# Performance work log

Measured on AMD Instinct MI355X. Metric: run time of the kernel, lower is better.

The kernel has to match this reference:

```python
import jax, jax.numpy as jnp
import numpy as np

PI = np.float32(np.pi)

def _normalize(x, eps=1e-6):
    # matches torch F.normalize: x / max(||x||, eps)
    return x / jnp.maximum(jnp.linalg.norm(x, axis=-1, keepdims=True), eps)

def _linear2srgb(x, eps=1e-8):
    lin = 12.92 * x
    exp = 1.055 * jnp.power(jnp.maximum(x, eps), 1.0 / 2.4) - 0.055
    return jnp.where(x <= 0.0031308, lin, exp)

def _ggx_specular(nrm, surf2c, surf2l, roughness, fresnel):
    # nrm [N,3], surf2c [N,3], surf2l [1,L,3] (unit), roughness [N,1], fresnel [N,3]
    L = _normalize(surf2l)                                  # [1,L,3]
    V = _normalize(surf2c)                                  # [N,3]
    H = _normalize((L + V[:, None, :]) / 2.0)               # [N,L,3]
    N = _normalize(nrm)                                     # [N,3]
    NoV = jnp.sum(V * N, axis=-1, keepdims=True)            # [N,1]
    N = N * jnp.sign(NoV)
    NoL = jnp.clip(jnp.sum(N[:, None, :] * L, axis=-1, keepdims=True), 1e-6, 1.0)  # [N,L,1]
    NoV = jnp.clip(jnp.sum(N * V, axis=-1, keepdims=True), 1e-6, 1.0)              # [N,1]
    NoH = jnp.clip(jnp.sum(N[:, None, :] * H, axis=-1, keepdims=True), 1e-6, 1.0)  # [N,L,1]
    VoH = jnp.clip(jnp.sum(V[:, None, :] * H, axis=-1, keepdims=True), 1e-6, 1.0)  # [N,L,1]
    alpha = roughness * roughness                            # [N,1]
    alpha2 = alpha * alpha
    k = (alpha + 2.0 * roughness + 1.0) / 8.0                # [N,1]
    FMi = ((-5.55473) * VoH - 6.98316) * VoH                 # [N,L,1]
    frac0 = fresnel[:, None, :] + (1.0 - fresnel[:, None, :]) * jnp.power(2.0, FMi)  # [N,L,3]
    frac = frac0 * alpha2[:, None, :]                        # [N,L,3]
    nom0 = NoH * NoH * (alpha2[:, None, :] - 1.0) + 1.0      # [N,L,1]
    nom1 = NoV[:, None, :] * (1.0 - k[:, None, :]) + k[:, None, :]  # [N,1,1]
    nom2 = NoL * (1.0 - k[:, None, :]) + k[:, None, :]       # [N,L,1]
    nom = jnp.clip(4.0 * PI * nom0 * nom0 * nom1 * nom2, 1e-6, 4.0 * PI)
    return frac / nom                                        # [N,L,3]

def setup_inputs() -> dict:
    key = jax.random.key(0)
    ks = jax.random.split(key, 9)
    N, L = 32768, 512
    f32 = jnp.float32
    return {
        'viewdirs': jax.random.normal(ks[0], (N, 3), f32),
        'albedo': jax.random.uniform(ks[1], (N, 3), dtype=f32),
        'roughness': jax.random.uniform(ks[2], (N, 1), dtype=f32),
        'fresnel': jnp.full((N, 3), 0.04, dtype=f32),
        'normal': jax.random.normal(ks[3], (N, 3), f32),
        'light_dirs': jax.random.normal(ks[4], (L, 3), f32),
        'light_area_weight': jax.random.uniform(ks[5], (L,), dtype=f32),
        'env_rgbs': jax.random.uniform(ks[6], (L, 3), dtype=f32),
        'visibility': jax.random.uniform(ks[7], (N, L, 1), dtype=f32),
        'indirect_light': jax.random.uniform(ks[8], (N, L, 3), dtype=f32),
    }

def reference(viewdirs, albedo, roughness, fresnel, normal, light_dirs,
              light_area_weight, env_rgbs, visibility, indirect_light):
    # sample(): albedo clamp, roughness affine+clamp, normal normalize
    albedo = jnp.clip(albedo, 0.0, 1.0)
    roughness = jnp.clip(roughness * 0.9 + 0.09, 0.0, 1.0)
    nrm = _normalize(normal)
    surf2l = _normalize(light_dirs)[None, :, :]              # [1,L,3]
    surf2c = _normalize(-viewdirs)                            # [N,3]
    cosine = jnp.clip(jnp.einsum('lk,nk->nl', _normalize(light_dirs), nrm), 0.0)  # [N,L]
    mask = (cosine > 1e-6)[..., None]                         # [N,L,1]
    vis = visibility * mask                                   # scatter-into-zeros equivalent
    ind = indirect_light * mask
    spec = _ggx_specular(nrm, surf2c, surf2l, roughness, fresnel)  # [N,L,3]
    brdf = albedo[:, None, :] / PI + spec                      # [N,L,3]
    direct = env_rgbs[None, :, :]                              # [1,L,3] (light_idx all zero)
    w = cosine[..., None] * light_area_weight[None, :, None]   # [N,L,1]
    light_rgbs = vis * direct + ind
    rgb = _linear2srgb(jnp.clip(jnp.sum(brdf * light_rgbs * w, axis=1), 0.0, 1.0))
    wo_indir = _linear2srgb(jnp.sum(brdf * (vis * direct) * w, axis=1))
    wo_vis = _linear2srgb(jnp.sum(brdf * direct * w, axis=1))
    indir = _linear2srgb(jnp.sum(brdf * ind * w, axis=1))
    return rgb, wo_indir, wo_vis, indir
```

## Files before the change

kernel.cpp:

```cpp
#include <hip/hip_runtime.h>
#include <math.h>


#define PI_F     3.14159265358979323846f
#define FOURPI_F (4.0f * PI_F)
#define MAXL     512

__device__ __forceinline__ float fast_rcp(float x)  { float r; asm("v_rcp_f32 %0, %1" : "=v"(r) : "v"(x)); return r; }
__device__ __forceinline__ float fast_rsq(float x)  { float r; asm("v_rsq_f32 %0, %1" : "=v"(r) : "v"(x)); return r; }
__device__ __forceinline__ float fast_exp2(float x) { float r; asm("v_exp_f32 %0, %1" : "=v"(r) : "v"(x)); return r; }
__device__ __forceinline__ float fast_log2(float x) { float r; asm("v_log_f32 %0, %1" : "=v"(r) : "v"(x)); return r; }

__device__ __forceinline__ float lin2srgb(float x) {
  float lin = 12.92f * x;
  float xe  = fmaxf(x, 1e-8f);
  float e   = 1.055f * fast_exp2(fast_log2(xe) * (1.0f / 2.4f)) - 0.055f;
  return (x <= 0.0031308f) ? lin : e;
}

__device__ __forceinline__ float clamp01(float x) { return fminf(fmaxf(x, 0.0f), 1.0f); }
__device__ __forceinline__ float clampe(float x)  { return fminf(fmaxf(x, 1e-6f), 1.0f); }

template <int LC>
__global__ void __launch_bounds__(256)
tensoir_render(const float* __restrict__ viewdirs,
               const float* __restrict__ albedo,
               const float* __restrict__ roughness,
               const float* __restrict__ fresnel,
               const float* __restrict__ normal,
               const float* __restrict__ light_dirs,
               const float* __restrict__ law,
               const float* __restrict__ env_rgbs,
               const float* __restrict__ visibility,
               const float* __restrict__ indirect,
               float* __restrict__ out,
               int N, int Lrt) {
  __shared__ float4 s_ld[MAXL];
  __shared__ float4 s_env[MAXL];

  const int L = LC ? LC : Lrt;
  const int tid = threadIdx.x;
  const int lane = tid & 63;
  int n = blockIdx.x * 4 + (tid >> 6);
  if (n >= N) n = N - 1;

  float vx = -viewdirs[3 * n + 0], vy = -viewdirs[3 * n + 1], vz = -viewdirs[3 * n + 2];
  float nx = normal[3 * n + 0], ny = normal[3 * n + 1], nz = normal[3 * n + 2];
  float rough0 = roughness[n];
  const float fr = fresnel[3 * n + 0], fg = fresnel[3 * n + 1], fb = fresnel[3 * n + 2];
  float ar0 = albedo[3 * n + 0], ag0 = albedo[3 * n + 1], ab0 = albedo[3 * n + 2];

  for (int l = tid; l < L && l < MAXL; l += 256) {
    float lx = light_dirs[3 * l + 0];
    float ly = light_dirs[3 * l + 1];
    float lz = light_dirs[3 * l + 2];
    float inv = fast_rsq(fmaxf(lx * lx + ly * ly + lz * lz, 1e-12f));
    s_ld[l]  = make_float4(lx * inv, ly * inv, lz * inv, law[l]);
    s_env[l] = make_float4(env_rgbs[3 * l + 0], env_rgbs[3 * l + 1],
                           env_rgbs[3 * l + 2], 0.0f);
  }
  __syncthreads();

  {
    float inv = fast_rsq(fmaxf(vx * vx + vy * vy + vz * vz, 1e-12f));
    vx *= inv; vy *= inv; vz *= inv;
  }
  {
    float inv = fast_rsq(fmaxf(nx * nx + ny * ny + nz * nz, 1e-12f));
    nx *= inv; ny *= inv; nz *= inv;
  }
  const float rough  = clamp01(rough0 * 0.9f + 0.09f);
  const float alpha  = rough * rough;
  const float alpha2 = alpha * alpha;
  const float a2m1   = alpha2 - 1.0f;
  const float kk     = (alpha + 2.0f * rough + 1.0f) * 0.125f;
  const float onemk  = 1.0f - kk;

  const float omfr = 1.0f - fr, omfg = 1.0f - fg, omfb = 1.0f - fb;
  const float ar = clamp01(ar0) * (1.0f / PI_F);
  const float ag = clamp01(ag0) * (1.0f / PI_F);
  const float ab = clamp01(ab0) * (1.0f / PI_F);

  const float NoV0 = vx * nx + vy * ny + vz * nz;
  const float sgn  = (NoV0 >= 0.0f) ? 1.0f : -1.0f;
  const float aNoV = fabsf(NoV0);
  const float NoV  = clampe(aNoV);
  const float nom1 = NoV * onemk + kk;
  const float c1   = FOURPI_F * nom1;

  float s1r = 0, s1g = 0, s1b = 0;
  float s2r = 0, s2g = 0, s2b = 0;
  float s3r = 0, s3g = 0, s3b = 0;

  const float* visrow = visibility + (size_t)n * L;
  const float* indrow = indirect + (size_t)n * L * 3;

  auto body = [&](int i) {
    const float4 ld = s_ld[i];
    const float4 ev = s_env[i];
    const float visv = visrow[i];
    const float ir = indrow[3 * i + 0];
    const float ig = indrow[3 * i + 1];
    const float ib = indrow[3 * i + 2];

    const float cos0 = ld.x * nx + ld.y * ny + ld.z * nz;
    const float LoV  = ld.x * vx + ld.y * vy + ld.z * vz;

    const float cosine = fmaxf(cos0, 0.0f);
    const bool  mask   = cos0 > 1e-6f;
    const float w      = cosine * ld.w;

    const float NoL0 = sgn * cos0;
    const float NoL  = clampe(NoL0);

    const float h2   = fmaf(2.0f, LoV, 2.0f);
    const float hinv = fast_rsq(fmaxf(h2, 1e-12f));
    const float VoH  = clampe((1.0f + LoV) * hinv);
    const float NoH  = clampe((NoL0 + aNoV) * hinv);

    const float FMi = (-5.55473f * VoH - 6.98316f) * VoH;
    const float p2  = fast_exp2(FMi);
    const float nom0 = fmaf(NoH * NoH, a2m1, 1.0f);
    const float nom2 = fmaf(NoL, onemk, kk);
    const float nom  = fminf(fmaxf(c1 * (nom0 * nom0) * nom2, 1e-6f), FOURPI_F);
    const float ss   = alpha2 * fast_rcp(nom);

    const float br = fmaf(fmaf(omfr, p2, fr), ss, ar);
    const float bg = fmaf(fmaf(omfg, p2, fg), ss, ag);
    const float bb = fmaf(fmaf(omfb, p2, fb), ss, ab);

    const float vism = mask ? visv : 0.0f;
    const float irm  = mask ? ir : 0.0f;
    const float igm  = mask ? ig : 0.0f;
    const float ibm  = mask ? ib : 0.0f;

    const float twr = br * w, twg = bg * w, twb = bb * w;

    s1r = fmaf(twr, vism * ev.x, s1r);
    s1g = fmaf(twg, vism * ev.y, s1g);
    s1b = fmaf(twb, vism * ev.z, s1b);
    s2r = fmaf(twr, ev.x, s2r);
    s2g = fmaf(twg, ev.y, s2g);
    s2b = fmaf(twb, ev.z, s2b);
    s3r = fmaf(twr, irm, s3r);
    s3g = fmaf(twg, igm, s3g);
    s3b = fmaf(twb, ibm, s3b);
  };

  if (LC) {
    constexpr int NITER = LC ? LC / 64 : 1;
#pragma unroll
    for (int j = 0; j < NITER; ++j) body(lane + 64 * j);
  } else {
    for (int i = lane; i < L; i += 64) body(i);
  }

#define WAVE_RED(v)                 \
  do {                              \
    v += __shfl_xor(v, 32);         \
    v += __shfl_xor(v, 16);         \
    v += __shfl_xor(v, 8);          \
    v += __shfl_xor(v, 4);          \
    v += __shfl_xor(v, 2);          \
    v += __shfl_xor(v, 1);          \
  } while (0)
  WAVE_RED(s1r); WAVE_RED(s1g); WAVE_RED(s1b);
  WAVE_RED(s2r); WAVE_RED(s2g); WAVE_RED(s2b);
  WAVE_RED(s3r); WAVE_RED(s3g); WAVE_RED(s3b);
#undef WAVE_RED

  if (lane == 0) {
    const size_t stride = (size_t)3 * N;
    float* o0 = out + 3 * (size_t)n;
    float* o1 = o0 + stride;
    float* o2 = o1 + stride;
    float* o3 = o2 + stride;
    o0[0] = lin2srgb(clamp01(s1r + s3r));
    o0[1] = lin2srgb(clamp01(s1g + s3g));
    o0[2] = lin2srgb(clamp01(s1b + s3b));
    o1[0] = lin2srgb(s1r); o1[1] = lin2srgb(s1g); o1[2] = lin2srgb(s1b);
    o2[0] = lin2srgb(s2r); o2[1] = lin2srgb(s2g); o2[2] = lin2srgb(s2b);
    o3[0] = lin2srgb(s3r); o3[1] = lin2srgb(s3g); o3[2] = lin2srgb(s3b);
  }
}

extern "C" void kernel_launch(void* const* d_in, const int* in_sizes, int n_in,
                              void* d_out, int out_size, void* d_ws, size_t ws_size,
                              hipStream_t stream) {
  const float* viewdirs   = (const float*)d_in[0];
  const float* albedo     = (const float*)d_in[1];
  const float* roughness  = (const float*)d_in[2];
  const float* fresnel    = (const float*)d_in[3];
  const float* normal     = (const float*)d_in[4];
  const float* light_dirs = (const float*)d_in[5];
  const float* law        = (const float*)d_in[6];
  const float* env_rgbs   = (const float*)d_in[7];
  const float* visibility = (const float*)d_in[8];
  const float* indirect   = (const float*)d_in[9];
  float* out = (float*)d_out;

  const int N = in_sizes[0] / 3;
  const int L = in_sizes[6];

  dim3 block(256);
  dim3 grid((N + 3) / 4);

  if (L == 512) {
    hipLaunchKernelGGL(tensoir_render<512>, grid, block, 0, stream,
                       viewdirs, albedo, roughness, fresnel, normal,
                       light_dirs, law, env_rgbs, visibility, indirect,
                       out, N, L);
  } else {
    hipLaunchKernelGGL(tensoir_render<0>, grid, block, 0, stream,
                       viewdirs, albedo, roughness, fresnel, normal,
                       light_dirs, law, env_rgbs, visibility, indirect,
                       out, N, L);
  }
}
```

Measured before the change: 52.71 us.

## Precompute normalized light table in a prep kernel and drop per-block LDS staging

Adds a small prep kernel that normalizes light directions and packs them with area weights and env colors into float4 tables in the workspace. The main kernel now reads these tables from global memory (L1/L2 cached) instead of each of 8192 blocks recomputing them into shared memory behind a __syncthreads. This removes redundant per-block setup work and the barrier, and frees LDS that may raise occupancy. The trade-offs are an extra kernel launch and per-lane global loads of the tables in the inner loop.

```diff
diff --git a/kernel.cpp b/kernel.cpp
--- a/kernel.cpp
+++ b/kernel.cpp
@@ -4,7 +4,6 @@
 
 #define PI_F     3.14159265358979323846f
 #define FOURPI_F (4.0f * PI_F)
-#define MAXL     512
 
 __device__ __forceinline__ float fast_rcp(float x)  { float r; asm("v_rcp_f32 %0, %1" : "=v"(r) : "v"(x)); return r; }
 __device__ __forceinline__ float fast_rsq(float x)  { float r; asm("v_rsq_f32 %0, %1" : "=v"(r) : "v"(x)); return r; }
@@ -20,6 +19,21 @@
 
 __device__ __forceinline__ float clamp01(float x) { return fminf(fmaxf(x, 0.0f), 1.0f); }
 __device__ __forceinline__ float clampe(float x)  { return fminf(fmaxf(x, 1e-6f), 1.0f); }
+
+__global__ void __launch_bounds__(256)
+prep_lights(const float* __restrict__ light_dirs, const float* __restrict__ law,
+            const float* __restrict__ env_rgbs, float4* __restrict__ ld_tbl,
+            float4* __restrict__ env_tbl, int L) {
+  int l = blockIdx.x * 256 + threadIdx.x;
+  if (l >= L) return;
+  float lx = light_dirs[3 * l + 0];
+  float ly = light_dirs[3 * l + 1];
+  float lz = light_dirs[3 * l + 2];
+  float inv = fast_rsq(fmaxf(lx * lx + ly * ly + lz * lz, 1e-12f));
+  ld_tbl[l]  = make_float4(lx * inv, ly * inv, lz * inv, law[l]);
+  env_tbl[l] = make_float4(env_rgbs[3 * l + 0], env_rgbs[3 * l + 1],
+                           env_rgbs[3 * l + 2], 0.0f);
+}
 
 template <int LC>
 __global__ void __launch_bounds__(256)
@@ -28,16 +42,12 @@
                const float* __restrict__ roughness,
                const float* __restrict__ fresnel,
                const float* __restrict__ normal,
-               const float* __restrict__ light_dirs,
-               const float* __restrict__ law,
-               const float* __restrict__ env_rgbs,
+               const float4* __restrict__ ld_tbl,
+               const float4* __restrict__ env_tbl,
                const float* __restrict__ visibility,
                const float* __restrict__ indirect,
                float* __restrict__ out,
                int N, int Lrt) {
-  __shared__ float4 s_ld[MAXL];
-  __shared__ float4 s_env[MAXL];
-
   const int L = LC ? LC : Lrt;
   const int tid = threadIdx.x;
   const int lane = tid & 63;
@@ -49,17 +59,6 @@
   float rough0 = roughness[n];
   const float fr = fresnel[3 * n + 0], fg = fresnel[3 * n + 1], fb = fresnel[3 * n + 2];
   float ar0 = albedo[3 * n + 0], ag0 = albedo[3 * n + 1], ab0 = albedo[3 * n + 2];
-
-  for (int l = tid; l < L && l < MAXL; l += 256) {
-    float lx = light_dirs[3 * l + 0];
-    float ly = light_dirs[3 * l + 1];
-    float lz = light_dirs[3 * l + 2];
-    float inv = fast_rsq(fmaxf(lx * lx + ly * ly + lz * lz, 1e-12f));
-    s_ld[l]  = make_float4(lx * inv, ly * inv, lz * inv, law[l]);
-    s_env[l] = make_float4(env_rgbs[3 * l + 0], env_rgbs[3 * l + 1],
-                           env_rgbs[3 * l + 2], 0.0f);
-  }
-  __syncthreads();
 
   {
     float inv = fast_rsq(fmaxf(vx * vx + vy * vy + vz * vz, 1e-12f));
@@ -96,8 +95,8 @@
   const float* indrow = indirect + (size_t)n * L * 3;
 
   auto body = [&](int i) {
-    const float4 ld = s_ld[i];
-    const float4 ev = s_env[i];
+    const float4 ld = ld_tbl[i];
+    const float4 ev = env_tbl[i];
     const float visv = visrow[i];
     const float ir = indrow[3 * i + 0];
     const float ig = indrow[3 * i + 1];
@@ -202,18 +201,24 @@
   const int N = in_sizes[0] / 3;
   const int L = in_sizes[6];
 
+  float4* ld_tbl  = (float4*)d_ws;
+  float4* env_tbl = ld_tbl + L;
+
+  hipLaunchKernelGGL(prep_lights, dim3((L + 255) / 256), dim3(256), 0, stream,
+                     light_dirs, law, env_rgbs, ld_tbl, env_tbl, L);
+
   dim3 block(256);
   dim3 grid((N + 3) / 4);
 
   if (L == 512) {
     hipLaunchKernelGGL(tensoir_render<512>, grid, block, 0, stream,
                        viewdirs, albedo, roughness, fresnel, normal,
-                       light_dirs, law, env_rgbs, visibility, indirect,
+                       ld_tbl, env_tbl, visibility, indirect,
                        out, N, L);
   } else {
     hipLaunchKernelGGL(tensoir_render<0>, grid, block, 0, stream,
                        viewdirs, albedo, roughness, fresnel, normal,
-                       light_dirs, law, env_rgbs, visibility, indirect,
+                       ld_tbl, env_tbl, visibility, indirect,
                        out, N, L);
   }
 }
```

Result: slower. 61.09 us (+15.9%).

## Remap threads so each lane owns a point and waves split lights

Applied to the files above, without the earlier changes.

For L=512 a new kernel assigns one point per lane (64 points per block), and the four waves each cover a 128-light slice. Each lane reads its own visibility and indirect rows with float4 loads, while light data is read from shared memory as wave-wide broadcasts. Partial sums are combined across waves through shared memory instead of shuffle reductions. The intent is to cut per-light shared-memory traffic and shuffle work. The cost is that global loads are now strided by a full row per lane rather than contiguous across the wave, which can hurt coalescing and DRAM efficiency on a bandwidth-bound kernel.

```diff
diff --git a/kernel.cpp b/kernel.cpp
--- a/kernel.cpp
+++ b/kernel.cpp
@@ -21,24 +21,181 @@
 __device__ __forceinline__ float clamp01(float x) { return fminf(fmaxf(x, 0.0f), 1.0f); }
 __device__ __forceinline__ float clampe(float x)  { return fminf(fmaxf(x, 1e-6f), 1.0f); }
 
-template <int LC>
+struct f3 { float x, y, z; };
+
 __global__ void __launch_bounds__(256)
-tensoir_render(const float* __restrict__ viewdirs,
-               const float* __restrict__ albedo,
-               const float* __restrict__ roughness,
-               const float* __restrict__ fresnel,
-               const float* __restrict__ normal,
-               const float* __restrict__ light_dirs,
-               const float* __restrict__ law,
-               const float* __restrict__ env_rgbs,
-               const float* __restrict__ visibility,
-               const float* __restrict__ indirect,
-               float* __restrict__ out,
-               int N, int Lrt) {
+tensoir_render64(const float* __restrict__ viewdirs,
+                 const float* __restrict__ albedo,
+                 const float* __restrict__ roughness,
+                 const float* __restrict__ fresnel,
+                 const float* __restrict__ normal,
+                 const float* __restrict__ light_dirs,
+                 const float* __restrict__ law,
+                 const float* __restrict__ env_rgbs,
+                 const float* __restrict__ visibility,
+                 const float* __restrict__ indirect,
+                 float* __restrict__ out, int N) {
+  constexpr int L = 512;
   __shared__ float4 s_ld[MAXL];
   __shared__ float4 s_env[MAXL];
-
-  const int L = LC ? LC : Lrt;
+  __shared__ float  red[9][4][64];
+
+  const int tid  = threadIdx.x;
+  const int lane = tid & 63;
+  const int wid  = tid >> 6;
+
+  for (int l = tid; l < L; l += 256) {
+    float lx = light_dirs[3 * l + 0];
+    float ly = light_dirs[3 * l + 1];
+    float lz = light_dirs[3 * l + 2];
+    float inv = fast_rsq(fmaxf(lx * lx + ly * ly + lz * lz, 1e-12f));
+    s_ld[l]  = make_float4(lx * inv, ly * inv, lz * inv, law[l]);
+    s_env[l] = make_float4(env_rgbs[3 * l + 0], env_rgbs[3 * l + 1],
+                           env_rgbs[3 * l + 2], 0.0f);
+  }
+  __syncthreads();
+
+  int n = blockIdx.x * 64 + lane;
+  if (n >= N) n = N - 1;
+
+  float vx = -viewdirs[3 * n + 0], vy = -viewdirs[3 * n + 1], vz = -viewdirs[3 * n + 2];
+  float nx = normal[3 * n + 0], ny = normal[3 * n + 1], nz = normal[3 * n + 2];
+  {
+    float inv = fast_rsq(fmaxf(vx * vx + vy * vy + vz * vz, 1e-12f));
+    vx *= inv; vy *= inv; vz *= inv;
+  }
+  {
+    float inv = fast_rsq(fmaxf(nx * nx + ny * ny + nz * nz, 1e-12f));
+    nx *= inv; ny *= inv; nz *= inv;
+  }
+  const float rough  = clamp01(roughness[n] * 0.9f + 0.09f);
+  const float alpha  = rough * rough;
+  const float alpha2 = alpha * alpha;
+  const float a2m1   = alpha2 - 1.0f;
+  const float kk     = (alpha + 2.0f * rough + 1.0f) * 0.125f;
+  const float onemk  = 1.0f - kk;
+
+  const float fr = fresnel[3 * n + 0], fg = fresnel[3 * n + 1], fb = fresnel[3 * n + 2];
+  const float omfr = 1.0f - fr, omfg = 1.0f - fg, omfb = 1.0f - fb;
+  const float ar = clamp01(albedo[3 * n + 0]) * (1.0f / PI_F);
+  const float ag = clamp01(albedo[3 * n + 1]) * (1.0f / PI_F);
+  const float ab = clamp01(albedo[3 * n + 2]) * (1.0f / PI_F);
+
+  const float NoV0 = vx * nx + vy * ny + vz * nz;
+  const float sgn  = (NoV0 >= 0.0f) ? 1.0f : -1.0f;
+  const float aNoV = fabsf(NoV0);
+  const float NoV  = clampe(aNoV);
+  const float nom1 = NoV * onemk + kk;
+  const float c1   = FOURPI_F * nom1;
+
+  float s1r = 0, s1g = 0, s1b = 0;
+  float s2r = 0, s2g = 0, s2b = 0;
+  float s3r = 0, s3g = 0, s3b = 0;
+
+  const float4* vis4 = (const float4*)(visibility + (size_t)n * L);
+  const float4* ind4 = (const float4*)(indirect + (size_t)n * L * 3);
+
+  const int l0 = wid * 128;
+
+#define LIGHT_BODY(ld, ev, visv, ir_, ig_, ib_)                                 \
+  do {                                                                          \
+    const float cos0 = (ld).x * nx + (ld).y * ny + (ld).z * nz;                 \
+    const float LoV  = (ld).x * vx + (ld).y * vy + (ld).z * vz;                 \
+    const float cosine = fmaxf(cos0, 0.0f);                                     \
+    const bool  mask   = cos0 > 1e-6f;                                          \
+    const float w      = cosine * (ld).w;                                       \
+    const float NoL0 = sgn * cos0;                                              \
+    const float NoL  = clampe(NoL0);                                            \
+    const float h2   = fmaf(2.0f, LoV, 2.0f);                                   \
+    const float hinv = fast_rsq(fmaxf(h2, 1e-12f));                             \
+    const float VoH  = clampe((1.0f + LoV) * hinv);                             \
+    const float NoH  = clampe((NoL0 + aNoV) * hinv);                            \
+    const float FMi = (-5.55473f * VoH - 6.98316f) * VoH;                       \
+    const float p2  = fast_exp2(FMi);                                           \
+    const float nom0 = fmaf(NoH * NoH, a2m1, 1.0f);                             \
+    const float nom2 = fmaf(NoL, onemk, kk);                                    \
+    const float nom  = fminf(fmaxf(c1 * (nom0 * nom0) * nom2, 1e-6f), FOURPI_F);\
+    const float ss   = alpha2 * fast_rcp(nom);                                  \
+    const float br = fmaf(fmaf(omfr, p2, fr), ss, ar);                          \
+    const float bg = fmaf(fmaf(omfg, p2, fg), ss, ag);                          \
+    const float bb = fmaf(fmaf(omfb, p2, fb), ss, ab);                          \
+    const float vism = mask ? (visv) : 0.0f;                                    \
+    const float irm  = mask ? (ir_) : 0.0f;                                     \
+    const float igm  = mask ? (ig_) : 0.0f;                                     \
+    const float ibm  = mask ? (ib_) : 0.0f;                                     \
+    const float twr = br * w, twg = bg * w, twb = bb * w;                       \
+    s1r = fmaf(twr, vism * (ev).x, s1r);                                        \
+    s1g = fmaf(twg, vism * (ev).y, s1g);                                        \
+    s1b = fmaf(twb, vism * (ev).z, s1b);                                        \
+    s2r = fmaf(twr, (ev).x, s2r);                                               \
+    s2g = fmaf(twg, (ev).y, s2g);                                               \
+    s2b = fmaf(twb, (ev).z, s2b);                                               \
+    s3r = fmaf(twr, irm, s3r);                                                  \
+    s3g = fmaf(twg, igm, s3g);                                                  \
+    s3b = fmaf(twb, ibm, s3b);                                                  \
+  } while (0)
+
+  for (int g = 0; g < 32; ++g) {
+    const int base = l0 + g * 4;
+    const float4 va = vis4[base >> 2];
+    const float4 i0 = ind4[(base >> 2) * 3 + 0];
+    const float4 i1 = ind4[(base >> 2) * 3 + 1];
+    const float4 i2 = ind4[(base >> 2) * 3 + 2];
+
+    const float4 d0 = s_ld[base + 0], e0 = s_env[base + 0];
+    const float4 d1 = s_ld[base + 1], e1 = s_env[base + 1];
+    const float4 d2 = s_ld[base + 2], e2 = s_env[base + 2];
+    const float4 d3 = s_ld[base + 3], e3 = s_env[base + 3];
+
+    LIGHT_BODY(d0, e0, va.x, i0.x, i0.y, i0.z);
+    LIGHT_BODY(d1, e1, va.y, i0.w, i1.x, i1.y);
+    LIGHT_BODY(d2, e2, va.z, i1.z, i1.w, i2.x);
+    LIGHT_BODY(d3, e3, va.w, i2.y, i2.z, i2.w);
+  }
+#undef LIGHT_BODY
+
+  red[0][wid][lane] = s1r; red[1][wid][lane] = s1g; red[2][wid][lane] = s1b;
+  red[3][wid][lane] = s2r; red[4][wid][lane] = s2g; red[5][wid][lane] = s2b;
+  red[6][wid][lane] = s3r; red[7][wid][lane] = s3g; red[8][wid][lane] = s3b;
+  __syncthreads();
+
+  if (wid == 0) {
+    float t[9];
+#pragma unroll
+    for (int s = 0; s < 9; ++s)
+      t[s] = red[s][0][lane] + red[s][1][lane] + red[s][2][lane] + red[s][3][lane];
+
+    const size_t stride = (size_t)3 * N;
+    float* o0 = out + 3 * (size_t)n;
+    float* o1 = o0 + stride;
+    float* o2 = o1 + stride;
+    float* o3 = o2 + stride;
+    f3 r0, r1, r2, r3;
+    r0.x = lin2srgb(clamp01(t[0] + t[6]));
+    r0.y = lin2srgb(clamp01(t[1] + t[7]));
+    r0.z = lin2srgb(clamp01(t[2] + t[8]));
+    r1.x = lin2srgb(t[0]); r1.y = lin2srgb(t[1]); r1.z = lin2srgb(t[2]);
+    r2.x = lin2srgb(t[3]); r2.y = lin2srgb(t[4]); r2.z = lin2srgb(t[5]);
+    r3.x = lin2srgb(t[6]); r3.y = lin2srgb(t[7]); r3.z = lin2srgb(t[8]);
+    *(f3*)o0 = r0; *(f3*)o1 = r1; *(f3*)o2 = r2; *(f3*)o3 = r3;
+  }
+}
+
+__global__ void __launch_bounds__(256)
+tensoir_render_generic(const float* __restrict__ viewdirs,
+                       const float* __restrict__ albedo,
+                       const float* __restrict__ roughness,
+                       const float* __restrict__ fresnel,
+                       const float* __restrict__ normal,
+                       const float* __restrict__ light_dirs,
+                       const float* __restrict__ law,
+                       const float* __restrict__ env_rgbs,
+                       const float* __restrict__ visibility,
+                       const float* __restrict__ indirect,
+                       float* __restrict__ out, int N, int L) {
+  __shared__ float4 s_ld[MAXL];
+  __shared__ float4 s_env[MAXL];
+
   const int tid = threadIdx.x;
   const int lane = tid & 63;
   int n = blockIdx.x * 4 + (tid >> 6);
@@ -75,12 +232,10 @@
   const float a2m1   = alpha2 - 1.0f;
   const float kk     = (alpha + 2.0f * rough + 1.0f) * 0.125f;
   const float onemk  = 1.0f - kk;
-
   const float omfr = 1.0f - fr, omfg = 1.0f - fg, omfb = 1.0f - fb;
   const float ar = clamp01(ar0) * (1.0f / PI_F);
   const float ag = clamp01(ag0) * (1.0f / PI_F);
   const float ab = clamp01(ab0) * (1.0f / PI_F);
-
   const float NoV0 = vx * nx + vy * ny + vz * nz;
   const float sgn  = (NoV0 >= 0.0f) ? 1.0f : -1.0f;
   const float aNoV = fabsf(NoV0);
@@ -95,47 +250,38 @@
   const float* visrow = visibility + (size_t)n * L;
   const float* indrow = indirect + (size_t)n * L * 3;
 
-  auto body = [&](int i) {
+  for (int i = lane; i < L; i += 64) {
     const float4 ld = s_ld[i];
     const float4 ev = s_env[i];
     const float visv = visrow[i];
     const float ir = indrow[3 * i + 0];
     const float ig = indrow[3 * i + 1];
     const float ib = indrow[3 * i + 2];
-
     const float cos0 = ld.x * nx + ld.y * ny + ld.z * nz;
     const float LoV  = ld.x * vx + ld.y * vy + ld.z * vz;
-
     const float cosine = fmaxf(cos0, 0.0f);
     const bool  mask   = cos0 > 1e-6f;
     const float w      = cosine * ld.w;
-
     const float NoL0 = sgn * cos0;
     const float NoL  = clampe(NoL0);
-
     const float h2   = fmaf(2.0f, LoV, 2.0f);
     const float hinv = fast_rsq(fmaxf(h2, 1e-12f));
     const float VoH  = clampe((1.0f + LoV) * hinv);
     const float NoH  = clampe((NoL0 + aNoV) * hinv);
-
     const float FMi = (-5.55473f * VoH - 6.98316f) * VoH;
     const float p2  = fast_exp2(FMi);
     const float nom0 = fmaf(NoH * NoH, a2m1, 1.0f);
     const float nom2 = fmaf(NoL, onemk, kk);
     const float nom  = fminf(fmaxf(c1 * (nom0 * nom0) * nom2, 1e-6f), FOURPI_F);
     const float ss   = alpha2 * fast_rcp(nom);
-
     const float br = fmaf(fmaf(omfr, p2, fr), ss, ar);
     const float bg = fmaf(fmaf(omfg, p2, fg), ss, ag);
     const float bb = fmaf(fmaf(omfb, p2, fb), ss, ab);
-
     const float vism = mask ? visv : 0.0f;
     const float irm  = mask ? ir : 0.0f;
     const float igm  = mask ? ig : 0.0f;
     const float ibm  = mask ? ib : 0.0f;
-
     const float twr = br * w, twg = bg * w, twb = bb * w;
-
     s1r = fmaf(twr, vism * ev.x, s1r);
     s1g = fmaf(twg, vism * ev.y, s1g);
     s1b = fmaf(twb, vism * ev.z, s1b);
@@ -145,14 +291,6 @@
     s3r = fmaf(twr, irm, s3r);
     s3g = fmaf(twg, igm, s3g);
     s3b = fmaf(twb, ibm, s3b);
-  };
-
-  if (LC) {
-    constexpr int NITER = LC ? LC / 64 : 1;
-#pragma unroll
-    for (int j = 0; j < NITER; ++j) body(lane + 64 * j);
-  } else {
-    for (int i = lane; i < L; i += 64) body(i);
   }
 
 #define WAVE_RED(v)                 \
@@ -203,17 +341,18 @@
   const int L = in_sizes[6];
 
   dim3 block(256);
-  dim3 grid((N + 3) / 4);
 
   if (L == 512) {
-    hipLaunchKernelGGL(tensoir_render<512>, grid, block, 0, stream,
+    const int blocks = (N + 63) / 64;
+    hipLaunchKernelGGL(tensoir_render64, dim3(blocks), block, 0, stream,
+                       viewdirs, albedo, roughness, fresnel, normal,
+                       light_dirs, law, env_rgbs, visibility, indirect,
+                       out, N);
+  } else {
+    const int blocks = (N + 3) / 4;
+    hipLaunchKernelGGL(tensoir_render_generic, dim3(blocks), block, 0, stream,
                        viewdirs, albedo, roughness, fresnel, normal,
                        light_dirs, law, env_rgbs, visibility, indirect,
                        out, N, L);
-  } else {
-    hipLaunchKernelGGL(tensoir_render<0>, grid, block, 0, stream,
-                       viewdirs, albedo, roughness, fresnel, normal,
-                       light_dirs, law, env_rgbs, visibility, indirect,
-                       out, N, L);
   }
 }
```

Result: slower. 125.7 us (+138.5%).
